# Kernel optimization log

Hardware: AMD Instinct MI355X
Metric: run time of the kernel (lower is better)

Reference implementation:

```python
import jax, jax.numpy as jnp
import numpy as np

# Config matching init_kwargs
N, C, H, W = 16, 256, 56, 56
O, KS, STRIDE, PAD = 512, 3, 1, 1
TABLE_SIZE, M_AUG = 16, 5
BUCKET = O // TABLE_SIZE            # fixed bucket size (32) for static shapes
SPAN = KS * KS * C                  # kernel_span = 2304


def _np_hash(a, v):
    # hf: abs(floor(a . v)) mod table_size  (matches fmod_ then abs_ on the torch side)
    return int(abs(np.floor(np.dot(a, v)))) % TABLE_SIZE


def setup_inputs() -> dict:
    rng = np.random.default_rng(0)
    stdv = 1.0 / np.sqrt(SPAN)
    kernels = rng.uniform(-stdv, stdv, (O, SPAN)).astype(np.float32)
    a = rng.standard_normal(SPAN + M_AUG).astype(np.float32)
    # _build_alsh_table: hash each kernel row via P(x,m) = concat(x, ||x||^2,...,||x||^(2^m))
    buckets = [[] for _ in range(TABLE_SIZE)]
    for r in range(O):
        k = kernels[r]
        nrm = float(np.linalg.norm(k))
        powers = np.array([nrm ** (2 ** (i + 1)) for i in range(M_AUG)], dtype=np.float32)
        buckets[_np_hash(a, np.concatenate([k, powers]))].append(r)
    # pack into equal-size buckets (overflow spills to the next bucket with space)
    # so that the selected-row count is static and jit-compatible.
    table = np.zeros((TABLE_SIZE, BUCKET), dtype=np.int32)
    fill = [0] * TABLE_SIZE
    overflow = []
    for b in range(TABLE_SIZE):
        for r in buckets[b]:
            if fill[b] < BUCKET:
                table[b, fill[b]] = r
                fill[b] += 1
            else:
                overflow.append(r)
    for r in overflow:
        for b in range(TABLE_SIZE):
            if fill[b] < BUCKET:
                table[b, fill[b]] = r
                fill[b] += 1
                break
    x = jax.random.normal(jax.random.key(0), (N, C, H, W), dtype=jnp.float32)
    return {"x": x, "kernels": jnp.asarray(kernels), "a": jnp.asarray(a),
            "table": jnp.asarray(table)}


def reference(x, kernels, a, table):
    h2 = (H - KS + 2 * PAD) // STRIDE + 1
    w2 = (W - KS + 2 * PAD) // STRIDE + 1
    # im2col: (kh*kw, N, C, h2, w2); stride=1 so plain slices suffice
    xp = jnp.pad(x, ((0, 0), (0, 0), (PAD, PAD), (PAD, PAD)))
    patches = jnp.stack([xp[:, :, i:i + h2, j:j + w2]
                         for i in range(KS) for j in range(KS)])
    # layout (kh, kw, C) along rows to match kernels.view(O, -1)
    pm = patches.transpose(0, 2, 1, 3, 4).reshape(SPAN, -1)  # (SPAN, N*h2*w2)
    # query: torch.rand(5).long() == 0, so the 5 "random" columns are all column 0
    col0 = pm[:, 0]
    unit = col0 / jnp.linalg.norm(col0)
    q = jnp.concatenate([unit, jnp.full((M_AUG,), 0.5, dtype=unit.dtype)])  # Q(x,m)
    idx = (jnp.abs(jnp.floor(jnp.dot(a, q))).astype(jnp.int32)) % TABLE_SIZE
    rows = table[idx]                       # (BUCKET,) selected kernel rows
    sub = kernels[rows] @ pm                # (BUCKET, N*h2*w2) subset matmul
    out = sub * (O / BUCKET)                # out /= rows.size/O
    out = out.reshape(BUCKET, N, h2 * w2).transpose(1, 0, 2)
    return out.reshape(N, BUCKET, h2, w2)
```

## Files before the change

### kernel.cpp

```cpp
#include <hip/hip_runtime.h>
#include <stdint.h>

#define C_IN 256
#define HW   56
#define HW2  3136
#define SPAN 2304
#define TS   16
#define BKT  32

typedef __attribute__((ext_vector_type(8)))  short short8;
typedef __attribute__((ext_vector_type(4)))  float f32x4;
typedef __attribute__((ext_vector_type(16))) float f32x16;
typedef float f32x4u __attribute__((ext_vector_type(4), aligned(4)));


__global__ void hash_rows_kernel(const float* __restrict__ x,
                                 const float* __restrict__ a,
                                 const int*   __restrict__ table,
                                 int*         __restrict__ rows_out) {
    __shared__ float rd[256];
    __shared__ float rn[256];
    const int t = threadIdx.x;
    float dv = 0.f, nq = 0.f;
    for (int k = t; k < SPAN; k += 256) {
        const int p = k >> 8;
        const int c = k & 255;
        const int i = p / 3, j = p % 3;
        float v = 0.f;
        if (i >= 1 && j >= 1) v = x[c * HW2 + (i - 1) * HW + (j - 1)];
        dv += a[k] * v;
        nq += v * v;
    }
    rd[t] = dv; rn[t] = nq;
    __syncthreads();
    for (int s = 128; s > 0; s >>= 1) {
        if (t < s) { rd[t] += rd[t + s]; rn[t] += rn[t + s]; }
        __syncthreads();
    }
    if (t == 0) {
        const float nrm = sqrtf(rn[0]);
        const float sv  = rd[0] / nrm
                        + 0.5f * (a[SPAN] + a[SPAN+1] + a[SPAN+2] + a[SPAN+3] + a[SPAN+4]);
        const int idx = ((int)fabsf(floorf(sv))) % TS;
        #pragma unroll
        for (int b = 0; b < BKT; ++b) rows_out[b] = table[idx * BKT + b];
    }
}

__global__ void build_wpack_kernel(const float* __restrict__ kernels,
                                   const int*   __restrict__ rows,
                                   unsigned short* __restrict__ wp) {
    const int idx   = blockIdx.x * 256 + threadIdx.x;
    const int j     = idx & 7;
    const int l     = (idx >> 3) & 63;
    const int Q     = idx >> 9;
    const int ccb   = Q / 18;
    const int rem   = Q % 18;
    const int p     = rem >> 1;
    const int ch16  = rem & 1;
    const int brow  = l & 31;
    const int khalf = l >> 5;
    const int k     = p * 256 + ccb * 32 + ch16 * 16 + khalf * 8 + j;
    const int row   = rows[brow];
    const float v = kernels[(size_t)row * SPAN + k] * 16.0f;
    unsigned u = __builtin_bit_cast(unsigned, v);
    u = (u + 0x7fffu + ((u >> 16) & 1u)) >> 16;
    wp[idx] = (unsigned short)u;
}

__global__ __launch_bounds__(512, 4)
void alsh_mfma_kernel(const float* __restrict__ x,
                      const unsigned short* __restrict__ wp,
                      float* __restrict__ out) {
    __shared__ float red[8 * 1024];

    const int b  = blockIdx.x;
    const int ct = (b & 7) * 196 + (b >> 3);

    const int t     = threadIdx.x;
    const int lane  = t & 63;
    const int wid   = t >> 6;
    const int ccb   = wid;
    const int col   = lane & 31;
    const int khalf = lane >> 5;
    const int s0    = ct * 32;
    const int n     = s0 / HW2;
    const int s0img = s0 - n * HW2;
    const int sl    = s0img + col;
    const int h     = sl / HW;
    const int w     = sl - h * HW;
    const float* xn = x + (size_t)n * (C_IN * HW2);
    const short8* wpv = (const short8*)wp;

    f32x16 acc = {0.f,0.f,0.f,0.f, 0.f,0.f,0.f,0.f, 0.f,0.f,0.f,0.f, 0.f,0.f,0.f,0.f};

    const int cc = ccb * 32;
    #pragma unroll
    for (int dd = 0; dd < 3; ++dd) {
        const int di     = dd - 1;
        const int rowpos = sl + di * HW;
        const int posm   = rowpos - 1;
        const int pc     = posm < 0 ? 0 : (posm > HW2 - 4 ? HW2 - 4 : posm);
        const bool shifted = (pc != posm);
        const int ih = h + di;

        #pragma unroll
        for (int ch16 = 0; ch16 < 2; ++ch16) {
            f32x4 V[8];
            #pragma unroll
            for (int j = 0; j < 8; ++j) {
                const int ch = cc + ch16 * 16 + khalf * 8 + j;
                V[j] = *(const f32x4u*)(xn + (size_t)ch * HW2 + pc);
            }

            #pragma unroll
            for (int dd2 = 0; dd2 < 3; ++dd2) {
                const int dj = dd2 - 1;
                const int iw = w + dj;
                const bool ok = ((unsigned)ih < (unsigned)HW) & ((unsigned)iw < (unsigned)HW);
                const int voff = rowpos + dj;

                short8 bf;
                #pragma unroll
                for (int j = 0; j < 8; ++j) {
                    float v = V[j][dd2];
                    if (shifted) {
                        const int vc = voff < 0 ? 0 : (voff > HW2 - 1 ? HW2 - 1 : voff);
                        v = xn[(size_t)(cc + ch16 * 16 + khalf * 8 + j) * HW2 + vc];
                    }
                    v = ok ? v : 0.f;
                    const unsigned u = __builtin_bit_cast(unsigned, v);
                    bf[j] = (short)((u + 0x8000u) >> 16);
                }

                const int Q = ccb * 18 + (dd * 3 + dd2) * 2 + ch16;
                const short8 a = wpv[Q * 64 + lane];
                acc = __builtin_amdgcn_mfma_f32_32x32x16_bf16(a, bf, acc, 0, 0, 0);
            }
        }
    }

    const int base = wid * 1024;
    #pragma unroll
    for (int i2 = 0; i2 < 16; ++i2) {
        const int b0 = (i2 & 3) + 8 * (i2 >> 2) + 4 * khalf;
        red[base + b0 * 32 + col] = acc[i2];
    }
    __syncthreads();

    float* on = out + (size_t)n * (BKT * HW2) + s0img;
    #pragma unroll
    for (int e = 0; e < 2; ++e) {
        const int elem = e * 512 + t;
        float s = red[elem];
        #pragma unroll
        for (int w2 = 1; w2 < 8; ++w2) s += red[w2 * 1024 + elem];
        const int b0 = elem >> 5;
        const int c  = elem & 31;
        on[(size_t)b0 * HW2 + c] = s;
    }
}

extern "C" void kernel_launch(void* const* d_in, const int* in_sizes, int n_in,
                              void* d_out, int out_size, void* d_ws, size_t ws_size,
                              hipStream_t stream) {
    const float* x       = (const float*)d_in[0];
    const float* kernels = (const float*)d_in[1];
    const float* a       = (const float*)d_in[2];
    const int*   table   = (const int*)d_in[3];
    float* out = (float*)d_out;
    int*   rows = (int*)d_ws;
    unsigned short* wpack = (unsigned short*)((char*)d_ws + 512);

    hipLaunchKernelGGL(hash_rows_kernel, dim3(1), dim3(256), 0, stream,
                       x, a, table, rows);
    hipLaunchKernelGGL(build_wpack_kernel, dim3(288), dim3(256), 0, stream,
                       kernels, rows, wpack);
    hipLaunchKernelGGL(alsh_mfma_kernel, dim3(1568), dim3(512), 0, stream,
                       x, wpack, out);
}
```

Before: 49.21 us.

## Pre-transpose input to channel-last bf16 before the MFMA conv kernel

Adds a transpose kernel that converts x from NCHW fp32 to per-position channel-contiguous bf16 in workspace. The MFMA kernel then loads one 16-byte short8 per tap directly, with no per-element conversion and no scattered strided loads. The cost is an extra launch plus a full write and re-read of a roughly 51 MB intermediate. It also depends on the workspace being large enough, and falls back to the old kernel otherwise.

```diff
diff --git a/kernel.cpp b/kernel.cpp
--- a/kernel.cpp
+++ b/kernel.cpp
@@ -9,10 +9,13 @@
 #define BKT  32
 
 typedef __attribute__((ext_vector_type(8)))  short short8;
+typedef __attribute__((ext_vector_type(8)))  unsigned short ushort8;
 typedef __attribute__((ext_vector_type(4)))  float f32x4;
 typedef __attribute__((ext_vector_type(16))) float f32x16;
 typedef float f32x4u __attribute__((ext_vector_type(4), aligned(4)));
 
+#define XT_OFF 262144
+#define XT_BYTES (16u * HW2 * 256u * 2u)
 
 __global__ void hash_rows_kernel(const float* __restrict__ x,
                                  const float* __restrict__ a,
@@ -68,15 +71,122 @@
     wp[idx] = (unsigned short)u;
 }
 
+__global__ __launch_bounds__(256)
+void transpose_kernel(const float* __restrict__ x,
+                      unsigned short* __restrict__ xT) {
+    __shared__ float tileF[32 * 257];
+    const int t  = threadIdx.x;
+    const int n  = blockIdx.x / 98;
+    const int p0 = (blockIdx.x % 98) * 32;
+    const float* xn = x + (size_t)n * (C_IN * HW2);
+
+    const int s4 = (t & 7) * 4;
+    const int c0 = t >> 3;
+    #pragma unroll
+    for (int iter = 0; iter < 8; ++iter) {
+        const int ch = iter * 32 + c0;
+        const f32x4 v = *(const f32x4*)(xn + (size_t)ch * HW2 + p0 + s4);
+        #pragma unroll
+        for (int j = 0; j < 4; ++j)
+            tileF[(s4 + j) * 257 + ch] = v[j];
+    }
+    __syncthreads();
+
+    const int pos = t >> 3;
+    const int cq  = t & 7;
+    unsigned short* dst = xT + ((size_t)n * HW2 + p0 + pos) * 256;
+    #pragma unroll
+    for (int iter = 0; iter < 4; ++iter) {
+        const int ch = iter * 64 + cq * 8;
+        ushort8 o;
+        #pragma unroll
+        for (int j = 0; j < 8; ++j) {
+            const unsigned u = __builtin_bit_cast(unsigned, tileF[pos * 257 + ch + j]);
+            o[j] = (unsigned short)((u + 0x8000u) >> 16);
+        }
+        *(ushort8*)(dst + ch) = o;
+    }
+}
+
 __global__ __launch_bounds__(512, 4)
-void alsh_mfma_kernel(const float* __restrict__ x,
-                      const unsigned short* __restrict__ wp,
-                      float* __restrict__ out) {
+void alsh_mfma_xt_kernel(const unsigned short* __restrict__ xT,
+                         const unsigned short* __restrict__ wp,
+                         float* __restrict__ out) {
     __shared__ float red[8 * 1024];
 
     const int b  = blockIdx.x;
     const int ct = (b & 7) * 196 + (b >> 3);
 
+    const int t     = threadIdx.x;
+    const int lane  = t & 63;
+    const int wid   = t >> 6;
+    const int ccb   = wid;
+    const int col   = lane & 31;
+    const int khalf = lane >> 5;
+    const int s0    = ct * 32;
+    const int n     = s0 / HW2;
+    const int s0img = s0 - n * HW2;
+    const int sl    = s0img + col;
+    const int h     = sl / HW;
+    const int w     = sl - h * HW;
+    const short8* xTn = (const short8*)(xT + (size_t)n * (HW2 * 256));
+    const short8* wpv = (const short8*)wp;
+
+    f32x16 acc = {0.f,0.f,0.f,0.f, 0.f,0.f,0.f,0.f, 0.f,0.f,0.f,0.f, 0.f,0.f,0.f,0.f};
+    const short8 z8 = {0,0,0,0,0,0,0,0};
+    const int ub = ccb * 4 + khalf;
+
+    #pragma unroll
+    for (int dd = 0; dd < 3; ++dd) {
+        const int di     = dd - 1;
+        const int rowpos = sl + di * HW;
+        const int ih     = h + di;
+        #pragma unroll
+        for (int ch16 = 0; ch16 < 2; ++ch16) {
+            #pragma unroll
+            for (int dd2 = 0; dd2 < 3; ++dd2) {
+                const int dj = dd2 - 1;
+                const int iw = w + dj;
+                const bool ok = ((unsigned)ih < (unsigned)HW) & ((unsigned)iw < (unsigned)HW);
+                const int voff = rowpos + dj;
+                const int vc = voff < 0 ? 0 : (voff > HW2 - 1 ? HW2 - 1 : voff);
+
+                short8 bv = xTn[(size_t)vc * 32 + ub + ch16 * 2];
+                bv = ok ? bv : z8;
+
+                const int Q = ccb * 18 + (dd * 3 + dd2) * 2 + ch16;
+                const short8 a = wpv[Q * 64 + lane];
+                acc = __builtin_amdgcn_mfma_f32_32x32x16_bf16(a, bv, acc, 0, 0, 0);
+            }
+        }
+    }
+
+    const int base = wid * 1024;
+    #pragma unroll
+    for (int i2 = 0; i2 < 16; ++i2) {
+        const int b0 = (i2 & 3) + 8 * (i2 >> 2) + 4 * khalf;
+        red[base + b0 * 32 + col] = acc[i2];
+    }
+    __syncthreads();
+
+    float* on = out + (size_t)n * (BKT * HW2) + s0img;
+    #pragma unroll
+    for (int e = 0; e < 2; ++e) {
+        const int elem = e * 512 + t;
+        float s = red[elem];
+        #pragma unroll
+        for (int w2 = 1; w2 < 8; ++w2) s += red[w2 * 1024 + elem];
+        on[(size_t)(elem >> 5) * HW2 + (elem & 31)] = s;
+    }
+}
+
+__global__ __launch_bounds__(512, 4)
+void alsh_mfma_reg_kernel(const float* __restrict__ x,
+                          const unsigned short* __restrict__ wp,
+                          float* __restrict__ out) {
+    __shared__ float red[8 * 1024];
+    const int b  = blockIdx.x;
+    const int ct = (b & 7) * 196 + (b >> 3);
     const int t     = threadIdx.x;
     const int lane  = t & 63;
     const int wid   = t >> 6;
@@ -91,9 +201,7 @@
     const int w     = sl - h * HW;
     const float* xn = x + (size_t)n * (C_IN * HW2);
     const short8* wpv = (const short8*)wp;
-
     f32x16 acc = {0.f,0.f,0.f,0.f, 0.f,0.f,0.f,0.f, 0.f,0.f,0.f,0.f, 0.f,0.f,0.f,0.f};
-
     const int cc = ccb * 32;
     #pragma unroll
     for (int dd = 0; dd < 3; ++dd) {
@@ -103,7 +211,6 @@
         const int pc     = posm < 0 ? 0 : (posm > HW2 - 4 ? HW2 - 4 : posm);
         const bool shifted = (pc != posm);
         const int ih = h + di;
-
         #pragma unroll
         for (int ch16 = 0; ch16 < 2; ++ch16) {
             f32x4 V[8];
@@ -112,14 +219,12 @@
                 const int ch = cc + ch16 * 16 + khalf * 8 + j;
                 V[j] = *(const f32x4u*)(xn + (size_t)ch * HW2 + pc);
             }
-
             #pragma unroll
             for (int dd2 = 0; dd2 < 3; ++dd2) {
                 const int dj = dd2 - 1;
                 const int iw = w + dj;
                 const bool ok = ((unsigned)ih < (unsigned)HW) & ((unsigned)iw < (unsigned)HW);
                 const int voff = rowpos + dj;
-
                 short8 bf;
                 #pragma unroll
                 for (int j = 0; j < 8; ++j) {
@@ -132,14 +237,12 @@
                     const unsigned u = __builtin_bit_cast(unsigned, v);
                     bf[j] = (short)((u + 0x8000u) >> 16);
                 }
-
                 const int Q = ccb * 18 + (dd * 3 + dd2) * 2 + ch16;
                 const short8 a = wpv[Q * 64 + lane];
                 acc = __builtin_amdgcn_mfma_f32_32x32x16_bf16(a, bf, acc, 0, 0, 0);
             }
         }
     }
-
     const int base = wid * 1024;
     #pragma unroll
     for (int i2 = 0; i2 < 16; ++i2) {
@@ -147,7 +250,6 @@
         red[base + b0 * 32 + col] = acc[i2];
     }
     __syncthreads();
-
     float* on = out + (size_t)n * (BKT * HW2) + s0img;
     #pragma unroll
     for (int e = 0; e < 2; ++e) {
@@ -155,9 +257,7 @@
         float s = red[elem];
         #pragma unroll
         for (int w2 = 1; w2 < 8; ++w2) s += red[w2 * 1024 + elem];
-        const int b0 = elem >> 5;
-        const int c  = elem & 31;
-        on[(size_t)b0 * HW2 + c] = s;
+        on[(size_t)(elem >> 5) * HW2 + (elem & 31)] = s;
     }
 }
 
@@ -169,13 +269,22 @@
     const float* a       = (const float*)d_in[2];
     const int*   table   = (const int*)d_in[3];
     float* out = (float*)d_out;
-    int*   rows = (int*)d_ws;
+    int*            rows  = (int*)d_ws;
     unsigned short* wpack = (unsigned short*)((char*)d_ws + 512);
 
     hipLaunchKernelGGL(hash_rows_kernel, dim3(1), dim3(256), 0, stream,
                        x, a, table, rows);
     hipLaunchKernelGGL(build_wpack_kernel, dim3(288), dim3(256), 0, stream,
                        kernels, rows, wpack);
-    hipLaunchKernelGGL(alsh_mfma_kernel, dim3(1568), dim3(512), 0, stream,
-                       x, wpack, out);
-}
+
+    if (ws_size >= (size_t)XT_OFF + XT_BYTES) {
+        unsigned short* xT = (unsigned short*)((char*)d_ws + XT_OFF);
+        hipLaunchKernelGGL(transpose_kernel, dim3(1568), dim3(256), 0, stream,
+                           x, xT);
+        hipLaunchKernelGGL(alsh_mfma_xt_kernel, dim3(1568), dim3(512), 0, stream,
+                           xT, wpack, out);
+    } else {
+        hipLaunchKernelGGL(alsh_mfma_reg_kernel, dim3(1568), dim3(512), 0, stream,
+                           x, wpack, out);
+    }
+}
```

After: 61.71 us. 1.25x slower.
